# Kernel tuning notes

Measured on AMD Instinct MI355X. Metric: run time of the kernel, lower is better.

The kernel has to match this reference:

```python
import jax, jax.numpy as jnp
import numpy as np

PC = 512      # proposal_channels == conv_channels
INCH = 512    # in_channels of branch
B = 8
T = 64        # pyramid level length (feat_t) at order=0
TF = 256      # frame_level_feature length (clip_length)
KERNELS = [8, 16, 8, 4, 2, 2, 2]  # ConPoolingKernal
CLC = 498     # feature_lastclass channels (CLC + 2 == 500)
GROUPS = 32


def _gn(x, gamma, beta):
    # GroupNorm(32, C) over [B, C, L]
    Bb, C, L = x.shape
    xg = x.reshape(Bb, GROUPS, C // GROUPS, L)
    m = xg.mean(axis=(2, 3), keepdims=True)
    v = xg.var(axis=(2, 3), keepdims=True)
    xn = ((xg - m) * jax.lax.rsqrt(v + 1e-5)).reshape(Bb, C, L)
    return xn * gamma[None, :, None] + beta[None, :, None]


def _c1(x, w, b):
    # Unit1D kernel_shape=1: pointwise conv
    return jnp.einsum('bct,oc->bot', x, w) + b[None, :, None]


def _bmp(feat, segs):
    # BoundaryMaxPooling: first C/2 channels max-pooled over segs[...,0:2],
    # second C/2 over segs[...,2:4] (inclusive integer ranges, clamped).
    Bb, C, L = feat.shape
    C2 = C // 2
    pos = jnp.arange(L)
    def pool(f, s, e):
        s = jnp.clip(s, 0, L - 1)
        e = jnp.maximum(jnp.clip(e, 0, L - 1), s)
        mask = (pos[None, None, :] >= s[..., None]) & (pos[None, None, :] <= e[..., None])  # [B,T,L]
        return jnp.max(jnp.where(mask[:, None], f[:, :, None, :], -jnp.inf), axis=-1)  # [B,C2,T]
    return jnp.concatenate([pool(feat[:, :C2], segs[..., 0], segs[..., 1]),
                            pool(feat[:, C2:], segs[..., 2], segs[..., 3])], axis=1)


def _anchor_gather(feat, anc, K):
    # Vectorized per-anchor clamp/slice + nearest F.interpolate(size=K):
    # src index for output k of a slice [l, r] is l + floor(k * (r - l + 1) / K).
    Bb, C, L = feat.shape
    left = jnp.clip(anc[..., 0], 0, L)
    right = jnp.clip(anc[..., 1], 0, L)
    valid = right > left                      # empty slices -> zeros (torch branch)
    seglen = right + 1 - left
    k = jnp.arange(K)
    idx = jnp.clip(left[..., None] + (k[None, None, :] * seglen[..., None]) // K, 0, L - 1)  # [B,T,K]
    g = jax.vmap(lambda f, ix: f[:, ix])(feat, idx)   # [B,C,T,K]
    return g * valid[:, None, :, None].astype(feat.dtype)


def setup_inputs() -> dict:
    key = jax.random.key(0)
    ks = jax.random.split(key, 16)
    f32 = jnp.float32
    s = 0.02
    def w(k, shape):
        return jax.random.normal(k, shape, f32) * s
    inp = {}
    inp['feature'] = jax.random.normal(ks[0], (B, INCH, T), f32)
    inp['frame_level_feature'] = jax.random.normal(ks[1], (B, PC, TF), f32)
    inp['segments'] = jax.random.randint(ks[2], (B, T, 4), 0, T).astype(jnp.int32)
    inp['frame_segments'] = jax.random.randint(ks[3], (B, T, 4), 0, TF).astype(jnp.int32)
    inp['feature_lastclass'] = jax.random.normal(ks[4], (B, CLC, T), f32)
    inp['anchor'] = jnp.sort(jax.random.randint(ks[5], (B, T, 2), 0, T), axis=-1).astype(jnp.int32)
    inp['frame_anchor'] = jnp.sort(jax.random.randint(ks[6], (B, T, 2), 0, TF), axis=-1).astype(jnp.int32)
    inp['order'] = 0
    inp['LocResult_feature'] = jax.random.normal(ks[7], (B, 2, T), f32)
    inp['w_cur'] = w(ks[8], (PC, INCH)); inp['b_cur'] = jnp.zeros((PC,), f32)
    inp['g_cur'] = jnp.ones((PC,), f32); inp['be_cur'] = jnp.zeros((PC,), f32)
    inp['w_lr'] = w(ks[9], (2 * PC, INCH)); inp['b_lr'] = jnp.zeros((2 * PC,), f32)
    inp['g_lr'] = jnp.ones((2 * PC,), f32); inp['be_lr'] = jnp.zeros((2 * PC,), f32)
    inp['w_roi'] = w(ks[10], (PC, PC)); inp['b_roi'] = jnp.zeros((PC,), f32)
    inp['g_roi'] = jnp.ones((PC,), f32); inp['be_roi'] = jnp.zeros((PC,), f32)
    K1 = KERNELS[1]; K0 = KERNELS[0]
    inp['w_cp'] = w(ks[11], (PC, 2 * PC, K1)); inp['b_cp'] = jnp.zeros((PC,), f32)
    inp['w_cp0'] = w(ks[12], (PC, PC, K0)); inp['b_cp0'] = jnp.zeros((PC,), f32)
    CIN = 6 * PC + 500
    inp['w_prop'] = w(ks[13], (INCH, CIN)); inp['b_prop'] = jnp.zeros((INCH,), f32)
    inp['g_prop'] = jnp.ones((INCH,), f32); inp['be_prop'] = jnp.zeros((INCH,), f32)
    return inp


def reference(feature, frame_level_feature, segments, frame_segments, feature_lastclass,
              anchor, frame_anchor, order, LocResult_feature,
              w_cur, b_cur, g_cur, be_cur, w_lr, b_lr, g_lr, be_lr,
              w_roi, b_roi, g_roi, be_roi, w_cp, b_cp, w_cp0, b_cp0,
              w_prop, b_prop, g_prop, be_prop):
    relu = jax.nn.relu
    fm_short = relu(_gn(_c1(feature, w_cur, b_cur), g_cur, be_cur))           # [B,PC,T]
    feat_lr = relu(_gn(_c1(feature, w_lr, b_lr), g_lr, be_lr))                # [B,2PC,T]
    prop_feature = _bmp(feat_lr, segments)                                    # [B,2PC,T]
    prop_roi = relu(_gn(_c1(_bmp(frame_level_feature, frame_segments), w_roi, b_roi), g_roi, be_roi))
    K1 = KERNELS[order + 1]
    K0 = KERNELS[0]
    g1 = _anchor_gather(feat_lr, anchor, K1)                                  # [B,2PC,T,K1]
    con_feature = jnp.einsum('bctk,ock->bot', g1, w_cp) + b_cp[None, :, None]  # valid conv K1->1
    g0 = _anchor_gather(frame_level_feature, frame_anchor, K0)                # [B,PC,T,K0]
    frame_con = jnp.einsum('bctk,ock->bot', g0, w_cp0) + b_cp0[None, :, None]
    prop_con = relu(_gn(_c1(frame_con, w_roi, b_roi), g_roi, be_roi))
    cat = jnp.concatenate([prop_roi, prop_feature, fm_short, feature_lastclass,
                           con_feature, prop_con, LocResult_feature], axis=1)  # [B,6PC+500,T]
    out = relu(_gn(_c1(cat, w_prop, b_prop), g_prop, be_prop))                # [B,INCH,T]
    return (out, feat_lr)
```

## Files before the change

### kernel.cpp

```cpp
#include <hip/hip_runtime.h>
#include <math.h>

#define BB 8
#define CATP 3584
#define CAT_REAL 3572

typedef __attribute__((ext_vector_type(8))) short short8;
typedef __attribute__((ext_vector_type(4))) float f32x4;

__device__ inline ushort f2bf(float f) {
  union { float f; unsigned u; } x;
  x.f = f;
  return (ushort)((x.u + 0x7FFFu + ((x.u >> 16) & 1u)) >> 16);
}
__device__ inline float bf2f(unsigned us) {
  union { unsigned u; float f; } x;
  x.u = us << 16;
  return x.f;
}

template <int Cin, int Kf>
__device__ void cpT_tile(const float* __restrict__ W, ushort* __restrict__ D,
                         int nt, int cc) {
  const int tid = threadIdx.x;
  const int j = tid >> 6, l4 = (tid >> 4) & 3, l15 = tid & 15;
  const int o = nt * 64 + j * 16 + l15;
  const int cb = cc * 32 + l4 * 8;
  ushort rg[8][Kf];
#pragma unroll
  for (int q = 0; q < 8; q++) {
    const float* row = W + ((size_t)o * Cin + cb + q) * Kf;
#pragma unroll
    for (int kq = 0; kq < Kf / 4; kq++) {
      const float4 f = *(const float4*)(row + kq * 4);
      rg[q][kq * 4 + 0] = f2bf(f.x);
      rg[q][kq * 4 + 1] = f2bf(f.y);
      rg[q][kq * 4 + 2] = f2bf(f.z);
      rg[q][kq * 4 + 3] = f2bf(f.w);
    }
  }
#pragma unroll
  for (int k = 0; k < Kf; k++) {
    uint4 pk;
    pk.x = (unsigned)rg[0][k] | ((unsigned)rg[1][k] << 16);
    pk.y = (unsigned)rg[2][k] | ((unsigned)rg[3][k] << 16);
    pk.z = (unsigned)rg[4][k] | ((unsigned)rg[5][k] << 16);
    pk.w = (unsigned)rg[6][k] | ((unsigned)rg[7][k] << 16);
    *(uint4*)(D + ((size_t)(nt * Kf + k) * (Cin >> 5) + cc) * 2048 + tid * 8) = pk;
  }
}

__global__ __launch_bounds__(256) void prep_kernel(
    const float* __restrict__ w_cur, const float* __restrict__ w_lr,
    const float* __restrict__ w_roi, const float* __restrict__ w_prop,
    ushort* __restrict__ Wcomb, ushort* __restrict__ Wroi,
    ushort* __restrict__ Wprop, const float* __restrict__ w_cp,
    ushort* __restrict__ WcpT, const float* __restrict__ w_cp0,
    ushort* __restrict__ Wcp0T, const float* __restrict__ feature,
    const float* __restrict__ frame_feat, const float* __restrict__ lastcls,
    const float* __restrict__ locres, ushort* __restrict__ Ft,
    ushort* __restrict__ FfT, ushort* __restrict__ cat) {
  __shared__ float tile[64 * 65];
  const int bid = blockIdx.x;
  if (bid < 1408) {
    const int i = bid * 256 + threadIdx.x;
    const float* src;
    ushort* dst;
    int o, k8, Kc;
    bool pad = false;
    if (i < 98304) {
      o = i >> 6; k8 = i & 63; Kc = 16;
      src = (o < 512) ? (w_cur + (size_t)o * 512)
                      : (w_lr + (size_t)(o - 512) * 512);
      dst = Wcomb;
    } else if (i < 131072) {
      const int r = i - 98304;
      o = r >> 6; k8 = r & 63; Kc = 16;
      src = w_roi + (size_t)o * 512;
      dst = Wroi;
    } else {
      const int r = i - 131072;
      if (r >= 229376) return;
      o = r / 448; k8 = r % 448; Kc = 112;
      src = w_prop + (size_t)o * CAT_REAL;
      dst = Wprop;
      pad = true;
    }
    const int k = k8 * 8;
    float v[8];
    if (pad) {
#pragma unroll
      for (int q = 0; q < 8; q++) v[q] = (k + q < CAT_REAL) ? src[k + q] : 0.f;
    } else {
      const float4 f0 = *(const float4*)(src + k);
      const float4 f1 = *(const float4*)(src + k + 4);
      v[0] = f0.x; v[1] = f0.y; v[2] = f0.z; v[3] = f0.w;
      v[4] = f1.x; v[5] = f1.y; v[6] = f1.z; v[7] = f1.w;
    }
    uint4 pk;
    pk.x = (unsigned)f2bf(v[0]) | ((unsigned)f2bf(v[1]) << 16);
    pk.y = (unsigned)f2bf(v[2]) | ((unsigned)f2bf(v[3]) << 16);
    pk.z = (unsigned)f2bf(v[4]) | ((unsigned)f2bf(v[5]) << 16);
    pk.w = (unsigned)f2bf(v[6]) | ((unsigned)f2bf(v[7]) << 16);
    const int ot = o >> 6, ii = (o >> 4) & 3, l15 = o & 15;
    const int kc = k8 >> 2, l4 = k8 & 3;
    const size_t flat =
        ((((size_t)ot * Kc + kc) * 4 + ii) * 64 + l4 * 16 + l15) * 8;
    *(uint4*)(dst + flat) = pk;
    return;
  }
  if (bid < 1792) {
    const int local = bid - 1408;
    if (local < 256)
      cpT_tile<1024, 16>(w_cp, WcpT, local >> 5, local & 31);
    else {
      const int r = local - 256;
      cpT_tile<512, 8>(w_cp0, Wcp0T, r >> 4, r & 15);
    }
    return;
  }
  const int local = bid - 1792;
  const float* src;
  ushort* dst;
  int Cr, Cw, L, rs, co, cblk, lblk, b;
  if (local < 64) {
    src = feature; dst = Ft; Cr = 512; Cw = 512; L = 64; rs = 512; co = 0;
    cblk = local & 7; lblk = 0; b = local >> 3;
  } else if (local < 320) {
    const int r = local - 64;
    src = frame_feat; dst = FfT; Cr = 512; Cw = 512; L = 256; rs = 512; co = 0;
    cblk = r & 7; lblk = (r >> 3) & 3; b = r >> 5;
  } else if (local < 384) {
    const int r = local - 320;
    src = lastcls; dst = cat; Cr = 498; Cw = 498; L = 64; rs = CATP; co = 2048;
    cblk = r & 7; lblk = 0; b = r >> 3;
  } else {
    const int r = local - 384;
    src = locres; dst = cat; Cr = 2; Cw = 14; L = 64; rs = CATP; co = 3570;
    cblk = 0; lblk = 0; b = r;
  }
  const int c0 = cblk * 64, l0 = lblk * 64;
  for (int e = threadIdx.x; e < 4096; e += 256) {
    const int cc = e >> 6, ll = e & 63;
    const int c = c0 + cc;
    tile[cc * 65 + ll] = (c < Cr) ? src[((size_t)b * Cr + c) * L + l0 + ll] : 0.f;
  }
  __syncthreads();
  for (int e = threadIdx.x; e < 4096; e += 256) {
    const int ll = e >> 6, cc = e & 63;
    const int c = c0 + cc;
    if (c < Cw)
      dst[((size_t)b * L + l0 + ll) * rs + co + c] = f2bf(tile[cc * 65 + ll]);
  }
}

__device__ void gemm_gn_body(const ushort* __restrict__ Xt,
                             const ushort* __restrict__ Wb,
                             const float* __restrict__ bias,
                             const float* __restrict__ gamma,
                             const float* __restrict__ beta, int Kp,
                             int cpgShift, float* __restrict__ outF, int outFM,
                             ushort* __restrict__ catOut, int catStride,
                             int chOff, int ot, int b, float* smem) {
  float* red = smem;
  float* rs = smem + 4224;
  float* rss = smem + 4228;
  float* gmean = smem + 4232;
  float* grstd = smem + 4236;
  const int w = threadIdx.x >> 6;
  const int lane = threadIdx.x & 63;
  const int l15 = lane & 15, l4 = lane >> 4;
  const int o0 = ot * 64;
  const int wk = Kp >> 2;
  const int kbeg = w * wk, kend = kbeg + wk;

  f32x4 acc[4][4] = {};
  const ushort* wbase = Wb + (size_t)ot * (Kp >> 5) * 2048 + lane * 8;
  const ushort* bp[4];
#pragma unroll
  for (int j = 0; j < 4; j++)
    bp[j] = Xt + (size_t)(b * 64 + j * 16 + l15) * Kp + l4 * 8;

  for (int k = kbeg; k < kend; k += 32) {
    const int kc = k >> 5;
    short8 a[4], x[4];
#pragma unroll
    for (int i = 0; i < 4; i++)
      a[i] = *(const short8*)(wbase + ((size_t)kc * 4 + i) * 512);
#pragma unroll
    for (int j = 0; j < 4; j++) x[j] = *(const short8*)(bp[j] + k);
#pragma unroll
    for (int i = 0; i < 4; i++)
#pragma unroll
      for (int j = 0; j < 4; j++)
        acc[i][j] = __builtin_amdgcn_mfma_f32_16x16x32_bf16(a[i], x[j],
                                                            acc[i][j], 0, 0, 0);
  }

  for (int ww = 0; ww < 4; ww++) {
    __syncthreads();
    if (w == ww) {
#pragma unroll
      for (int i = 0; i < 4; i++)
#pragma unroll
        for (int j = 0; j < 4; j++)
#pragma unroll
          for (int r = 0; r < 4; r++) {
            const int m = i * 16 + l4 * 4 + r;
            const int n = j * 16 + l15;
            if (ww == 0)
              red[m * 65 + n] = acc[i][j][r] + bias[o0 + m];
            else
              red[m * 65 + n] += acc[i][j][r];
          }
    }
  }
  __syncthreads();

  const int cpg = 1 << cpgShift;
  const int ngroups = 64 >> cpgShift;
  for (int gi = 0; gi < ngroups; gi++) {
    float s = 0.f, ss = 0.f;
    const int nel = cpg << 6;
    for (int e = threadIdx.x; e < nel; e += 256) {
      const float v = red[((gi << cpgShift) + (e >> 6)) * 65 + (e & 63)];
      s += v;
      ss += v * v;
    }
#pragma unroll
    for (int off = 32; off > 0; off >>= 1) {
      s += __shfl_down(s, off);
      ss += __shfl_down(ss, off);
    }
    if (lane == 0) { rs[w] = s; rss[w] = ss; }
    __syncthreads();
    if (threadIdx.x == 0) {
      const float ts = rs[0] + rs[1] + rs[2] + rs[3];
      const float tss = rss[0] + rss[1] + rss[2] + rss[3];
      const float mean = ts / (float)nel;
      const float var = tss / (float)nel - mean * mean;
      gmean[gi] = mean;
      grstd[gi] = rsqrtf(var + 1e-5f);
    }
    __syncthreads();
  }

  if (outF) {
    for (int e = threadIdx.x; e < 4096; e += 256) {
      const int m = e >> 6, n = e & 63;
      const int gi = m >> cpgShift;
      const int c = o0 + m;
      float v = (red[m * 65 + n] - gmean[gi]) * grstd[gi] * gamma[c] + beta[c];
      v = fmaxf(v, 0.f);
      outF[((size_t)b * outFM + c) * 64 + n] = v;
    }
  }
  if (catOut) {
    for (int e = threadIdx.x; e < 4096; e += 256) {
      const int n = e >> 6, m = e & 63;
      const int gi = m >> cpgShift;
      const int c = o0 + m;
      float v = (red[m * 65 + n] - gmean[gi]) * grstd[gi] * gamma[c] + beta[c];
      v = fmaxf(v, 0.f);
      catOut[((size_t)(b * 64) + n) * catStride + chOff + c] = f2bf(v);
    }
  }
}

__device__ void gemm_part_body(const ushort* __restrict__ Xt,
                               const ushort* __restrict__ Wb,
                               float* __restrict__ P, int ot, int b, int slice,
                               int kc0, int kc1, float* red) {
  const int w = threadIdx.x >> 6;
  const int lane = threadIdx.x & 63;
  const int l15 = lane & 15, l4 = lane >> 4;

  f32x4 acc[4][4] = {};
  const ushort* wbase = Wb + (size_t)ot * (CATP >> 5) * 2048 + lane * 8;
  const ushort* bp[4];
#pragma unroll
  for (int j = 0; j < 4; j++)
    bp[j] = Xt + (size_t)(b * 64 + j * 16 + l15) * CATP + l4 * 8;

  for (int kc = kc0 + w; kc < kc1; kc += 4) {
    short8 a[4], x[4];
#pragma unroll
    for (int i = 0; i < 4; i++)
      a[i] = *(const short8*)(wbase + ((size_t)kc * 4 + i) * 512);
#pragma unroll
    for (int j = 0; j < 4; j++) x[j] = *(const short8*)(bp[j] + kc * 32);
#pragma unroll
    for (int i = 0; i < 4; i++)
#pragma unroll
      for (int j = 0; j < 4; j++)
        acc[i][j] = __builtin_amdgcn_mfma_f32_16x16x32_bf16(a[i], x[j],
                                                            acc[i][j], 0, 0, 0);
  }

  for (int ww = 0; ww < 4; ww++) {
    __syncthreads();
    if (w == ww) {
#pragma unroll
      for (int i = 0; i < 4; i++)
#pragma unroll
        for (int j = 0; j < 4; j++)
#pragma unroll
          for (int r = 0; r < 4; r++) {
            const int m = i * 16 + l4 * 4 + r;
            const int n = j * 16 + l15;
            if (ww == 0)
              red[m * 65 + n] = acc[i][j][r];
            else
              red[m * 65 + n] += acc[i][j][r];
          }
    }
  }
  __syncthreads();
  float* Pp = P + (((size_t)slice * BB + b) * 512 + ot * 64) * 64;
  for (int e = threadIdx.x; e < 4096; e += 256)
    Pp[e] = red[(e >> 6) * 65 + (e & 63)];
}

__global__ __launch_bounds__(256) void reduce_gn_kernel(
    const ushort* __restrict__ cat, const ushort* __restrict__ Wprop,
    const float* __restrict__ P, const float* __restrict__ bias,
    const float* __restrict__ gamma, const float* __restrict__ beta,
    float* __restrict__ outF) {
  const int ot = blockIdx.x;
  const int b = blockIdx.y;
  const int o0 = ot * 64;
  const int w = threadIdx.x >> 6;
  const int lane = threadIdx.x & 63;
  const int l15 = lane & 15, l4 = lane >> 4;

  f32x4 acc[4][4] = {};
  const ushort* wbase = Wprop + (size_t)ot * (CATP >> 5) * 2048 + lane * 8;
  const ushort* bp[4];
#pragma unroll
  for (int j = 0; j < 4; j++)
    bp[j] = cat + (size_t)(b * 64 + j * 16 + l15) * CATP + l4 * 8;

  for (int kc = 79 + w; kc < 112; kc += 4) {
    short8 a[4], x[4];
#pragma unroll
    for (int i = 0; i < 4; i++)
      a[i] = *(const short8*)(wbase + ((size_t)kc * 4 + i) * 512);
#pragma unroll
    for (int j = 0; j < 4; j++) x[j] = *(const short8*)(bp[j] + kc * 32);
#pragma unroll
    for (int i = 0; i < 4; i++)
#pragma unroll
      for (int j = 0; j < 4; j++)
        acc[i][j] = __builtin_amdgcn_mfma_f32_16x16x32_bf16(a[i], x[j],
                                                            acc[i][j], 0, 0, 0);
  }

  __shared__ float red[64 * 65];
  for (int ww = 0; ww < 4; ww++) {
    __syncthreads();
    if (w == ww) {
#pragma unroll
      for (int i = 0; i < 4; i++)
#pragma unroll
        for (int j = 0; j < 4; j++)
#pragma unroll
          for (int r = 0; r < 4; r++) {
            const int m = i * 16 + l4 * 4 + r;
            const int n = j * 16 + l15;
            if (ww == 0)
              red[m * 65 + n] = acc[i][j][r];
            else
              red[m * 65 + n] += acc[i][j][r];
          }
    }
  }
  __syncthreads();
  for (int e = threadIdx.x; e < 4096; e += 256) {
    const int m = e >> 6, n = e & 63;
    float s = bias[o0 + m];
#pragma unroll
    for (int z = 0; z < 3; z++)
      s += P[(((size_t)z * BB + b) * 512 + o0 + m) * 64 + n];
    red[m * 65 + n] += s;
  }
  __syncthreads();
  __shared__ float rs[4], rss[4], gmean[4], grstd[4];
  for (int gi = 0; gi < 4; gi++) {
    float s = 0.f, ss = 0.f;
    for (int e = threadIdx.x; e < 1024; e += 256) {
      const float v = red[((gi << 4) + (e >> 6)) * 65 + (e & 63)];
      s += v;
      ss += v * v;
    }
#pragma unroll
    for (int off = 32; off > 0; off >>= 1) {
      s += __shfl_down(s, off);
      ss += __shfl_down(ss, off);
    }
    if (lane == 0) { rs[w] = s; rss[w] = ss; }
    __syncthreads();
    if (threadIdx.x == 0) {
      const float ts = rs[0] + rs[1] + rs[2] + rs[3];
      const float tss = rss[0] + rss[1] + rss[2] + rss[3];
      const float mean = ts / 1024.f;
      const float var = tss / 1024.f - mean * mean;
      gmean[gi] = mean;
      grstd[gi] = rsqrtf(var + 1e-5f);
    }
    __syncthreads();
  }
  for (int e = threadIdx.x; e < 4096; e += 256) {
    const int m = e >> 6, n = e & 63;
    const int gi = m >> 4;
    const int c = o0 + m;
    float v = (red[m * 65 + n] - gmean[gi]) * grstd[gi] * gamma[c] + beta[c];
    outF[((size_t)b * 512 + c) * 64 + n] = fmaxf(v, 0.f);
  }
}

template <int C, int L>
__device__ void bmp_body(const ushort* __restrict__ Xt,
                         const int* __restrict__ segs, ushort* __restrict__ Y,
                         int rowStride, int chOff, int t, int b,
                         float2 (*pmax)[512]) {
  constexpr int C2 = C / 2;
  constexpr int P2 = C2 / 2;
  constexpr int CH = P2 / 64;
  const int w = threadIdx.x >> 6;
  const int lane = threadIdx.x & 63;
  const int* sg = segs + ((size_t)b * 64 + t) * 4;
  const ushort* Xb = Xt + (size_t)b * L * C;
#pragma unroll
  for (int h = 0; h < 2; h++) {
    const int s = min(max(sg[2 * h], 0), L - 1);
    const int e = max(min(max(sg[2 * h + 1], 0), L - 1), s);
#pragma unroll
    for (int q = 0; q < CH; q++) {
      const int p = q * 64 + lane;
      const ushort* base = Xb + h * C2 + 2 * p;
      float a0 = -INFINITY, a1 = -INFINITY;
      float c0 = -INFINITY, c1 = -INFINITY;
      int l = s + w;
      for (; l + 4 <= e; l += 8) {
        const unsigned u0 = *(const unsigned*)(base + (size_t)l * C);
        const unsigned u1 = *(const unsigned*)(base + (size_t)(l + 4) * C);
        a0 = fmaxf(a0, bf2f(u0 & 0xffffu));
        a1 = fmaxf(a1, bf2f(u0 >> 16));
        c0 = fmaxf(c0, bf2f(u1 & 0xffffu));
        c1 = fmaxf(c1, bf2f(u1 >> 16));
      }
      if (l <= e) {
        const unsigned u0 = *(const unsigned*)(base + (size_t)l * C);
        a0 = fmaxf(a0, bf2f(u0 & 0xffffu));
        a1 = fmaxf(a1, bf2f(u0 >> 16));
      }
      pmax[w][h * P2 + p] = make_float2(fmaxf(a0, c0), fmaxf(a1, c1));
    }
  }
  __syncthreads();
  for (int idx = threadIdx.x; idx < 2 * P2; idx += 256) {
    float2 m = pmax[0][idx];
#pragma unroll
    for (int ww = 1; ww < 4; ww++) {
      const float2 v = pmax[ww][idx];
      m.x = fmaxf(m.x, v.x);
      m.y = fmaxf(m.y, v.y);
    }
    const unsigned o = (unsigned)f2bf(m.x) | ((unsigned)f2bf(m.y) << 16);
    *(unsigned*)(Y + ((size_t)(b * 64) + t) * rowStride + chOff + 2 * idx) = o;
  }
}

template <int Kf, int L, int Cin>
__device__ void anchor_mfma_body(const ushort* __restrict__ src,
                                 const int* __restrict__ anc,
                                 const ushort* __restrict__ Wt,
                                 float* __restrict__ P, int nt, int b,
                                 int slice, float* red) {
  const int w = threadIdx.x >> 6;
  const int lane = threadIdx.x & 63;
  const int l15 = lane & 15, l4 = lane >> 4;
  const int kz = slice >> 1, chalf = slice & 1;
  const int k = kz * 4 + w;
  const int cbase = chalf * (Cin / 2);

  const ushort* rp[4];
#pragma unroll
  for (int i = 0; i < 4; i++) {
    const int t = i * 16 + l15;
    const int a0 = anc[((size_t)b * 64 + t) * 2 + 0];
    const int a1 = anc[((size_t)b * 64 + t) * 2 + 1];
    const int left = min(max(a0, 0), L);
    const int right = min(max(a1, 0), L);
    const int seglen = right + 1 - left;
    const int ix = min(max(left + (k * seglen) / Kf, 0), L - 1);
    rp[i] = src + ((size_t)b * L + ix) * Cin + cbase + l4 * 8;
  }
  const ushort* wb = Wt + (size_t)(nt * Kf + k) * (Cin >> 5) * 2048 + lane * 8;

  f32x4 acc[4][4] = {};
  for (int c0 = 0; c0 < Cin / 2; c0 += 32) {
    const int cc = (cbase + c0) >> 5;
    short8 a[4], bb[4];
#pragma unroll
    for (int i = 0; i < 4; i++) a[i] = *(const short8*)(rp[i] + c0);
#pragma unroll
    for (int j = 0; j < 4; j++)
      bb[j] = *(const short8*)(wb + ((size_t)cc * 4 + j) * 512);
#pragma unroll
    for (int i = 0; i < 4; i++)
#pragma unroll
      for (int j = 0; j < 4; j++)
        acc[i][j] = __builtin_amdgcn_mfma_f32_16x16x32_bf16(a[i], bb[j],
                                                            acc[i][j], 0, 0, 0);
  }

  for (int ww = 0; ww < 4; ww++) {
    __syncthreads();
    if (w == ww) {
#pragma unroll
      for (int i = 0; i < 4; i++)
#pragma unroll
        for (int j = 0; j < 4; j++)
#pragma unroll
          for (int r = 0; r < 4; r++) {
            const int m = i * 16 + l4 * 4 + r;
            const int n = j * 16 + l15;
            if (ww == 0)
              red[m * 65 + n] = acc[i][j][r];
            else
              red[m * 65 + n] += acc[i][j][r];
          }
    }
  }
  __syncthreads();
  float* Pp = P + (((size_t)slice * BB + b) * 512 + nt * 64) * 64;
  for (int e = threadIdx.x; e < 4096; e += 256) {
    const int n = e >> 6, m = e & 63;
    Pp[e] = red[m * 65 + n];
  }
}

__device__ void anchor_reduce_body(const float* __restrict__ P, int ks,
                                   const float* __restrict__ bias,
                                   const int* __restrict__ anc, int L,
                                   ushort* __restrict__ Y, int rowStride,
                                   int chOff, int ot, int b, float* smem) {
  float* tile = smem;
  float* sval = smem + 4160;
  const int o0 = ot * 64;
  if (threadIdx.x < 64) {
    const int t = threadIdx.x;
    const int a0 = anc[((size_t)b * 64 + t) * 2 + 0];
    const int a1 = anc[((size_t)b * 64 + t) * 2 + 1];
    const int left = min(max(a0, 0), L);
    const int right = min(max(a1, 0), L);
    sval[t] = (right > left) ? 1.f : 0.f;
  }
  __syncthreads();
  for (int e = threadIdx.x; e < 4096; e += 256) {
    const int nl = e >> 6, m = e & 63;
    const int n = o0 + nl;
    float s = 0.f;
    for (int z = 0; z < ks; z++)
      s += P[(((size_t)z * BB + b) * 512 + n) * 64 + m];
    tile[nl * 65 + m] = s * sval[m] + bias[n];
  }
  __syncthreads();
  for (int e = threadIdx.x; e < 4096; e += 256) {
    const int m = e >> 6, nl = e & 63;
    Y[((size_t)(b * 64) + m) * rowStride + chOff + o0 + nl] =
        f2bf(tile[nl * 65 + m]);
  }
}

__global__ __launch_bounds__(256) void fused_B_kernel(
    const ushort* __restrict__ Ft, const ushort* __restrict__ Wcomb,
    const float* __restrict__ b_cur, const float* __restrict__ g_cur,
    const float* __restrict__ be_cur, ushort* __restrict__ cat,
    const float* __restrict__ b_lr, const float* __restrict__ g_lr,
    const float* __restrict__ be_lr, float* __restrict__ feat_lr,
    ushort* __restrict__ FlrT, const ushort* __restrict__ FfT,
    const int* __restrict__ frame_segs, ushort* __restrict__ XbmpT,
    const int* __restrict__ frame_anchor, const ushort* __restrict__ Wcp0T,
    float* __restrict__ P0) {
  __shared__ __align__(16) float smem[4240];
  const int bid = blockIdx.x;
  if (bid < 256) {
    const int nt = bid & 7, b = (bid >> 3) & 7, s = bid >> 6;
    anchor_mfma_body<8, 256, 512>(FfT, frame_anchor, Wcp0T, P0, nt, b, s, smem);
  } else if (bid < 448) {
    const int r = bid - 256;
    const int b = r / 24, ot24 = r % 24;
    if (ot24 < 8)
      gemm_gn_body(Ft, Wcomb, b_cur, g_cur, be_cur, 512, 4, nullptr, 0, cat,
                   CATP, 1536, ot24, b, smem);
    else
      gemm_gn_body(Ft, Wcomb + 512 * 512, b_lr, g_lr, be_lr, 512, 5, feat_lr,
                   1024, FlrT, 1024, 0, ot24 - 8, b, smem);
  } else {
    const int r = bid - 448;
    bmp_body<512, 256>(FfT, frame_segs, XbmpT, 512, 0, r & 63, r >> 6,
                       (float2(*)[512])smem);
  }
}

__global__ __launch_bounds__(256) void fused_C_kernel(
    const ushort* __restrict__ FlrT, const int* __restrict__ segments,
    ushort* __restrict__ cat, const int* __restrict__ anchor,
    const ushort* __restrict__ WcpT, float* __restrict__ P1,
    const float* __restrict__ P0, const float* __restrict__ b_cp0,
    const int* __restrict__ frame_anchor, ushort* __restrict__ FconT,
    const ushort* __restrict__ XbmpT, const ushort* __restrict__ Wroi,
    const float* __restrict__ b_roi, const float* __restrict__ g_roi,
    const float* __restrict__ be_roi) {
  __shared__ __align__(16) float smem[4240];
  const int bid = blockIdx.x;
  if (bid < 512) {
    const int nt = bid & 7, b = (bid >> 3) & 7, s = bid >> 6;
    anchor_mfma_body<16, 64, 1024>(FlrT, anchor, WcpT, P1, nt, b, s, smem);
  } else if (bid < 576) {
    const int r = bid - 512;
    gemm_gn_body(XbmpT, Wroi, b_roi, g_roi, be_roi, 512, 4, nullptr, 0, cat,
                 CATP, 0, r & 7, r >> 3, smem);
  } else if (bid < 640) {
    const int r = bid - 576;
    anchor_reduce_body(P0, 4, b_cp0, frame_anchor, 256, FconT, 512, 0, r & 7,
                       r >> 3, smem);
  } else {
    const int r = bid - 640;
    bmp_body<1024, 64>(FlrT, segments, cat, CATP, 512, r & 63, r >> 6,
                       (float2(*)[512])smem);
  }
}

__global__ __launch_bounds__(256) void fused_D_kernel(
    const ushort* __restrict__ cat, const ushort* __restrict__ Wprop,
    float* __restrict__ P9, const float* __restrict__ P1,
    const float* __restrict__ b_cp, const int* __restrict__ anchor,
    ushort* __restrict__ catw, const ushort* __restrict__ FconT,
    const ushort* __restrict__ Wroi, const float* __restrict__ b_roi,
    const float* __restrict__ g_roi, const float* __restrict__ be_roi) {
  __shared__ __align__(16) float smem[4240];
  const int bid = blockIdx.x;
  if (bid < 192) {
    const int s = bid >> 6, q = bid & 63;
    const int kc0 = (s == 0) ? 0 : (s == 1) ? 27 : 53;
    const int kc1 = (s == 0) ? 27 : (s == 1) ? 53 : 79;
    gemm_part_body(cat, Wprop, P9, q & 7, q >> 3, s, kc0, kc1, smem);
  } else if (bid < 256) {
    const int r = bid - 192;
    anchor_reduce_body(P1, 8, b_cp, anchor, 64, catw, CATP, 2546, r & 7,
                       r >> 3, smem);
  } else {
    const int r = bid - 256;
    gemm_gn_body(FconT, Wroi, b_roi, g_roi, be_roi, 512, 4, nullptr, 0, catw,
                 CATP, 3058, r & 7, r >> 3, smem);
  }
}

extern "C" void kernel_launch(void* const* d_in, const int* in_sizes, int n_in,
                              void* d_out, int out_size, void* d_ws,
                              size_t ws_size, hipStream_t stream) {
  const float* feature      = (const float*)d_in[0];
  const float* frame_feat   = (const float*)d_in[1];
  const int*   segments     = (const int*)d_in[2];
  const int*   frame_segs   = (const int*)d_in[3];
  const float* feat_lastcls = (const float*)d_in[4];
  const int*   anchor       = (const int*)d_in[5];
  const int*   frame_anchor = (const int*)d_in[6];
  const float* locres       = (const float*)d_in[8];
  const float* w_cur  = (const float*)d_in[9];
  const float* b_cur  = (const float*)d_in[10];
  const float* g_cur  = (const float*)d_in[11];
  const float* be_cur = (const float*)d_in[12];
  const float* w_lr   = (const float*)d_in[13];
  const float* b_lr   = (const float*)d_in[14];
  const float* g_lr   = (const float*)d_in[15];
  const float* be_lr  = (const float*)d_in[16];
  const float* w_roi  = (const float*)d_in[17];
  const float* b_roi  = (const float*)d_in[18];
  const float* g_roi  = (const float*)d_in[19];
  const float* be_roi = (const float*)d_in[20];
  const float* w_cp   = (const float*)d_in[21];
  const float* b_cp   = (const float*)d_in[22];
  const float* w_cp0  = (const float*)d_in[23];
  const float* b_cp0  = (const float*)d_in[24];
  const float* w_prop = (const float*)d_in[25];
  const float* b_prop = (const float*)d_in[26];
  const float* g_prop = (const float*)d_in[27];
  const float* be_prop= (const float*)d_in[28];

  float* out_main = (float*)d_out;
  float* feat_lr  = (float*)d_out + BB * 512 * 64;

  ushort* cat_t  = (ushort*)d_ws;
  ushort* Ft     = cat_t + 1835008;
  ushort* XbmpT  = Ft + 262144;
  ushort* FconT  = XbmpT + 262144;
  ushort* Wcomb  = FconT + 262144;
  ushort* Wroi   = Wcomb + 786432;
  ushort* Wprop  = Wroi + 262144;
  ushort* WcpT   = Wprop + 1835008;
  ushort* Wcp0T  = WcpT + 8388608;
  ushort* FlrT   = Wcp0T + 2097152;
  ushort* FfT    = FlrT + 524288;
  float*  P1     = (float*)(FfT + 1048576);
  float*  P0     = P1 + 2097152;
  float*  P9     = P0 + 1048576;

  prep_kernel<<<2184, 256, 0, stream>>>(
      w_cur, w_lr, w_roi, w_prop, Wcomb, Wroi, Wprop, w_cp, WcpT, w_cp0,
      Wcp0T, feature, frame_feat, feat_lastcls, locres, Ft, FfT, cat_t);

  fused_B_kernel<<<960, 256, 0, stream>>>(
      Ft, Wcomb, b_cur, g_cur, be_cur, cat_t, b_lr, g_lr, be_lr, feat_lr,
      FlrT, FfT, frame_segs, XbmpT, frame_anchor, Wcp0T, P0);

  fused_C_kernel<<<1152, 256, 0, stream>>>(
      FlrT, segments, cat_t, anchor, WcpT, P1, P0, b_cp0, frame_anchor, FconT,
      XbmpT, Wroi, b_roi, g_roi, be_roi);

  fused_D_kernel<<<320, 256, 0, stream>>>(
      cat_t, Wprop, P9, P1, b_cp, anchor, cat_t, FconT, Wroi, b_roi, g_roi,
      be_roi);

  reduce_gn_kernel<<<dim3(8, BB), 256, 0, stream>>>(
      cat_t, Wprop, P9, b_prop, g_prop, be_prop, out_main);
}
```

Before: 310.6 us.

## Regroup fused stage kernels by operation type into more launches

Splits the three heterogeneous fused kernels into five launches, each grouping blocks of a similar kind: the pointwise GEMM+GN, both boundary max-pools, both anchor MFMA convolutions plus the ROI GEMM, both anchor reductions, and the prop partial GEMM with the prop_con GEMM. Each anchor conv now runs alongside the other instead of next to unrelated work, which aims to balance per-launch work and reduce tail imbalance from mixing block types. The cost is two extra kernel launches and added serialization points between stages.

```diff
diff --git a/kernel.cpp b/kernel.cpp
--- a/kernel.cpp
+++ b/kernel.cpp
@@ -574,73 +574,81 @@
   }
 }
 
-__global__ __launch_bounds__(256) void fused_B_kernel(
+__global__ __launch_bounds__(256) void gemm_seg_kernel(
     const ushort* __restrict__ Ft, const ushort* __restrict__ Wcomb,
     const float* __restrict__ b_cur, const float* __restrict__ g_cur,
     const float* __restrict__ be_cur, ushort* __restrict__ cat,
     const float* __restrict__ b_lr, const float* __restrict__ g_lr,
     const float* __restrict__ be_lr, float* __restrict__ feat_lr,
-    ushort* __restrict__ FlrT, const ushort* __restrict__ FfT,
-    const int* __restrict__ frame_segs, ushort* __restrict__ XbmpT,
-    const int* __restrict__ frame_anchor, const ushort* __restrict__ Wcp0T,
-    float* __restrict__ P0) {
+    ushort* __restrict__ FlrT) {
   __shared__ __align__(16) float smem[4240];
-  const int bid = blockIdx.x;
-  if (bid < 256) {
-    const int nt = bid & 7, b = (bid >> 3) & 7, s = bid >> 6;
-    anchor_mfma_body<8, 256, 512>(FfT, frame_anchor, Wcp0T, P0, nt, b, s, smem);
-  } else if (bid < 448) {
-    const int r = bid - 256;
-    const int b = r / 24, ot24 = r % 24;
-    if (ot24 < 8)
-      gemm_gn_body(Ft, Wcomb, b_cur, g_cur, be_cur, 512, 4, nullptr, 0, cat,
-                   CATP, 1536, ot24, b, smem);
-    else
-      gemm_gn_body(Ft, Wcomb + 512 * 512, b_lr, g_lr, be_lr, 512, 5, feat_lr,
-                   1024, FlrT, 1024, 0, ot24 - 8, b, smem);
-  } else {
-    const int r = bid - 448;
-    bmp_body<512, 256>(FfT, frame_segs, XbmpT, 512, 0, r & 63, r >> 6,
-                       (float2(*)[512])smem);
-  }
-}
-
-__global__ __launch_bounds__(256) void fused_C_kernel(
+  const int r = blockIdx.x;
+  const int b = r / 24, ot24 = r % 24;
+  if (ot24 < 8)
+    gemm_gn_body(Ft, Wcomb, b_cur, g_cur, be_cur, 512, 4, nullptr, 0, cat,
+                 CATP, 1536, ot24, b, smem);
+  else
+    gemm_gn_body(Ft, Wcomb + 512 * 512, b_lr, g_lr, be_lr, 512, 5, feat_lr,
+                 1024, FlrT, 1024, 0, ot24 - 8, b, smem);
+}
+
+__global__ __launch_bounds__(256) void bmp_dual_kernel(
     const ushort* __restrict__ FlrT, const int* __restrict__ segments,
-    ushort* __restrict__ cat, const int* __restrict__ anchor,
+    ushort* __restrict__ cat, const ushort* __restrict__ FfT,
+    const int* __restrict__ frame_segs, ushort* __restrict__ XbmpT) {
+  __shared__ float2 pm[4][512];
+  if (blockIdx.z == 0)
+    bmp_body<1024, 64>(FlrT, segments, cat, CATP, 512, blockIdx.x, blockIdx.y,
+                       pm);
+  else
+    bmp_body<512, 256>(FfT, frame_segs, XbmpT, 512, 0, blockIdx.x, blockIdx.y,
+                       pm);
+}
+
+__global__ __launch_bounds__(256) void anchor_plus_kernel(
+    const ushort* __restrict__ FlrT, const int* __restrict__ anchor,
     const ushort* __restrict__ WcpT, float* __restrict__ P1,
-    const float* __restrict__ P0, const float* __restrict__ b_cp0,
-    const int* __restrict__ frame_anchor, ushort* __restrict__ FconT,
+    const ushort* __restrict__ FfT, const int* __restrict__ frame_anchor,
+    const ushort* __restrict__ Wcp0T, float* __restrict__ P0,
     const ushort* __restrict__ XbmpT, const ushort* __restrict__ Wroi,
     const float* __restrict__ b_roi, const float* __restrict__ g_roi,
-    const float* __restrict__ be_roi) {
+    const float* __restrict__ be_roi, ushort* __restrict__ cat) {
   __shared__ __align__(16) float smem[4240];
   const int bid = blockIdx.x;
   if (bid < 512) {
     const int nt = bid & 7, b = (bid >> 3) & 7, s = bid >> 6;
     anchor_mfma_body<16, 64, 1024>(FlrT, anchor, WcpT, P1, nt, b, s, smem);
-  } else if (bid < 576) {
-    const int r = bid - 512;
+  } else if (bid < 768) {
+    const int local = bid - 512;
+    const int nt = local & 7, b = (local >> 3) & 7, s = local >> 6;
+    anchor_mfma_body<8, 256, 512>(FfT, frame_anchor, Wcp0T, P0, nt, b, s, smem);
+  } else {
+    const int r = bid - 768;
     gemm_gn_body(XbmpT, Wroi, b_roi, g_roi, be_roi, 512, 4, nullptr, 0, cat,
                  CATP, 0, r & 7, r >> 3, smem);
-  } else if (bid < 640) {
-    const int r = bid - 576;
-    anchor_reduce_body(P0, 4, b_cp0, frame_anchor, 256, FconT, 512, 0, r & 7,
-                       r >> 3, smem);
-  } else {
-    const int r = bid - 640;
-    bmp_body<1024, 64>(FlrT, segments, cat, CATP, 512, r & 63, r >> 6,
-                       (float2(*)[512])smem);
-  }
-}
-
-__global__ __launch_bounds__(256) void fused_D_kernel(
+  }
+}
+
+__global__ __launch_bounds__(256) void anchor_reduce_dual_kernel(
+    const float* __restrict__ P1, const float* __restrict__ b_cp,
+    const int* __restrict__ anchor, ushort* __restrict__ cat,
+    const float* __restrict__ P0, const float* __restrict__ b_cp0,
+    const int* __restrict__ frame_anchor, ushort* __restrict__ FconT) {
+  __shared__ __align__(16) float smem[4240];
+  if (blockIdx.z == 0)
+    anchor_reduce_body(P1, 8, b_cp, anchor, 64, cat, CATP, 2546, blockIdx.x,
+                       blockIdx.y, smem);
+  else
+    anchor_reduce_body(P0, 4, b_cp0, frame_anchor, 256, FconT, 512, 0,
+                       blockIdx.x, blockIdx.y, smem);
+}
+
+__global__ __launch_bounds__(256) void propcon_part_kernel(
     const ushort* __restrict__ cat, const ushort* __restrict__ Wprop,
-    float* __restrict__ P9, const float* __restrict__ P1,
-    const float* __restrict__ b_cp, const int* __restrict__ anchor,
-    ushort* __restrict__ catw, const ushort* __restrict__ FconT,
+    float* __restrict__ P9, const ushort* __restrict__ FconT,
     const ushort* __restrict__ Wroi, const float* __restrict__ b_roi,
-    const float* __restrict__ g_roi, const float* __restrict__ be_roi) {
+    const float* __restrict__ g_roi, const float* __restrict__ be_roi,
+    ushort* __restrict__ catw) {
   __shared__ __align__(16) float smem[4240];
   const int bid = blockIdx.x;
   if (bid < 192) {
@@ -648,12 +656,8 @@
     const int kc0 = (s == 0) ? 0 : (s == 1) ? 27 : 53;
     const int kc1 = (s == 0) ? 27 : (s == 1) ? 53 : 79;
     gemm_part_body(cat, Wprop, P9, q & 7, q >> 3, s, kc0, kc1, smem);
-  } else if (bid < 256) {
+  } else {
     const int r = bid - 192;
-    anchor_reduce_body(P1, 8, b_cp, anchor, 64, catw, CATP, 2546, r & 7,
-                       r >> 3, smem);
-  } else {
-    const int r = bid - 256;
     gemm_gn_body(FconT, Wroi, b_roi, g_roi, be_roi, 512, 4, nullptr, 0, catw,
                  CATP, 3058, r & 7, r >> 3, smem);
   }
@@ -713,17 +717,22 @@
       w_cur, w_lr, w_roi, w_prop, Wcomb, Wroi, Wprop, w_cp, WcpT, w_cp0,
       Wcp0T, feature, frame_feat, feat_lastcls, locres, Ft, FfT, cat_t);
 
-  fused_B_kernel<<<960, 256, 0, stream>>>(
+  gemm_seg_kernel<<<192, 256, 0, stream>>>(
       Ft, Wcomb, b_cur, g_cur, be_cur, cat_t, b_lr, g_lr, be_lr, feat_lr,
-      FlrT, FfT, frame_segs, XbmpT, frame_anchor, Wcp0T, P0);
-
-  fused_C_kernel<<<1152, 256, 0, stream>>>(
-      FlrT, segments, cat_t, anchor, WcpT, P1, P0, b_cp0, frame_anchor, FconT,
-      XbmpT, Wroi, b_roi, g_roi, be_roi);
-
-  fused_D_kernel<<<320, 256, 0, stream>>>(
-      cat_t, Wprop, P9, P1, b_cp, anchor, cat_t, FconT, Wroi, b_roi, g_roi,
-      be_roi);
+      FlrT);
+
+  bmp_dual_kernel<<<dim3(64, BB, 2), 256, 0, stream>>>(
+      FlrT, segments, cat_t, FfT, frame_segs, XbmpT);
+
+  anchor_plus_kernel<<<832, 256, 0, stream>>>(
+      FlrT, anchor, WcpT, P1, FfT, frame_anchor, Wcp0T, P0, XbmpT, Wroi,
+      b_roi, g_roi, be_roi, cat_t);
+
+  anchor_reduce_dual_kernel<<<dim3(8, BB, 2), 256, 0, stream>>>(
+      P1, b_cp, anchor, cat_t, P0, b_cp0, frame_anchor, FconT);
+
+  propcon_part_kernel<<<256, 256, 0, stream>>>(
+      cat_t, Wprop, P9, FconT, Wroi, b_roi, g_roi, be_roi, cat_t);
 
   reduce_gn_kernel<<<dim3(8, BB), 256, 0, stream>>>(
       cat_t, Wprop, P9, b_prop, g_prop, be_prop, out_main);
```

After: 310.9 us. No clear change (+0.1%).
